# Optimization experiments

Hardware: AMD Instinct MI355X
Metric: run time of the kernel (lower is better)

Reference implementation:

```python
import jax, jax.numpy as jnp
import numpy as np

B, L, E, H = 2, 2048, 2048, 16
HD = E // H  # 128
ROPE_BASE = 10000.0


def setup_inputs() -> dict:
    key = jax.random.key(0)
    k1, k2, k3 = jax.random.split(key, 3)
    x = jax.random.normal(k1, (B, L, E), dtype=jnp.float32)
    position_ids = jnp.tile(jnp.arange(L, dtype=jnp.int32)[None, :], (B, 1))
    # Linear weights stored as [in, out] so y = x @ W + b (equals torch x @ W.T + b)
    W_attn = jax.random.normal(k2, (E, 3 * E), dtype=jnp.float32) * (1.0 / np.sqrt(E))
    b_attn = jnp.zeros((3 * E,), dtype=jnp.float32)
    W_proj = jax.random.normal(k3, (E, E), dtype=jnp.float32) * (1.0 / np.sqrt(E))
    b_proj = jnp.zeros((E,), dtype=jnp.float32)
    return {"x": x, "position_ids": position_ids, "W_attn": W_attn,
            "b_attn": b_attn, "W_proj": W_proj, "b_proj": b_proj}


def _rotate_half(t):
    h = t.shape[-1] // 2
    return jnp.concatenate([-t[..., h:], t[..., :h]], axis=-1)


def _apply_rope(q, k, position_ids):
    # q,k: [B,H,L,HD]; position_ids: [B,L]
    inv_freq = 1.0 / (ROPE_BASE ** (jnp.arange(0, HD, 2, dtype=jnp.float32) / HD))
    angles = position_ids.astype(jnp.float32)[:, :, None] * inv_freq  # [B,L,HD/2]
    cos = jnp.concatenate([jnp.cos(angles)] * 2, axis=-1)[:, None]  # [B,1,L,HD]
    sin = jnp.concatenate([jnp.sin(angles)] * 2, axis=-1)[:, None]
    return q * cos + _rotate_half(q) * sin, k * cos + _rotate_half(k) * sin


def reference(x, position_ids, W_attn, b_attn, W_proj, b_proj):
    # fused QKV projection
    qkv = x @ W_attn + b_attn                       # [B,L,3E]
    q, k, v = jnp.split(qkv, 3, axis=-1)            # each [B,L,E]
    reshape = lambda t: t.reshape(B, L, H, HD).transpose(0, 2, 1, 3)  # [B,H,L,HD]
    q, k, v = reshape(q), reshape(k), reshape(v)
    q, k = _apply_rope(q, k, position_ids)
    # scaled dot-product attention (mask=None -> full attention, dropout 0)
    scores = jnp.einsum('bhqd,bhkd->bhqk', q, k) * (1.0 / np.sqrt(HD))
    probs = jax.nn.softmax(scores, axis=-1)
    y = jnp.einsum('bhqk,bhkd->bhqd', probs, v)     # [B,H,L,HD]
    y = y.transpose(0, 2, 1, 3).reshape(B, L, E)
    return y @ W_proj + b_proj
```

## Files before the change

kernel.cpp:

```cpp
#include <hip/hip_runtime.h>
#include <math.h>

#define BB 2
#define LL 2048
#define EE 2048
#define HH 16
#define HD 128
#define N3E (3*EE)

typedef __attribute__((ext_vector_type(8))) short  bf16x8;
typedef __attribute__((ext_vector_type(4))) float  f32x4;

__device__ __forceinline__ ushort f2bf(float f) {
    union { float f; unsigned u; } v; v.f = f;
    unsigned u = v.u + 0x7FFFu + ((v.u >> 16) & 1u);
    return (ushort)(u >> 16);
}
__device__ __forceinline__ float bf2f(ushort u) {
    union { unsigned u; float f; } v; v.u = ((unsigned)u) << 16;
    return v.f;
}

__global__ __launch_bounds__(256) void cvt_bf16(const float* __restrict__ in,
                                                ushort* __restrict__ out, int n) {
    int i = (blockIdx.x * 256 + threadIdx.x) * 8;
    float4 a = *(const float4*)(in + i);
    float4 b = *(const float4*)(in + i + 4);
    ushort4 p0 = { f2bf(a.x), f2bf(a.y), f2bf(a.z), f2bf(a.w) };
    ushort4 p1 = { f2bf(b.x), f2bf(b.y), f2bf(b.z), f2bf(b.w) };
    *(ushort4*)(out + i)     = p0;
    *(ushort4*)(out + i + 4) = p1;
}

__global__ __launch_bounds__(256) void transpose_bf16(const float* __restrict__ in,
                                                      ushort* __restrict__ out,
                                                      int R, int Ccol) {
    __shared__ float tile[32][33];
    int c0 = blockIdx.x * 32, r0 = blockIdx.y * 32;
    int t = threadIdx.x;
    int lr = t >> 5, lc = t & 31;
    #pragma unroll
    for (int i = 0; i < 4; ++i)
        tile[lr + i * 8][lc] = in[(size_t)(r0 + lr + i * 8) * Ccol + c0 + lc];
    __syncthreads();
    #pragma unroll
    for (int i = 0; i < 4; ++i)
        out[(size_t)(c0 + lr + i * 8) * R + r0 + lc] = f2bf(tile[lc][lr + i * 8]);
}

template<int WRITE_BF16>
__global__ __launch_bounds__(512, 2) void gemm_ktile(const ushort* __restrict__ A,
                                                     const ushort* __restrict__ Bt,
                                                     const float* __restrict__ bias,
                                                     void* __restrict__ C,
                                                     int M, int N, int K, int nbx) {
    __shared__ __align__(16) ushort Asl[4 * 8192];
    __shared__ __align__(16) ushort Bsl[4 * 4096];

    const int t    = threadIdx.x;
    const int lane = t & 63;
    const int w    = t >> 6;
    const int m    = lane & 15;
    const int quad = lane >> 4;
    const int wm   = w >> 1;
    const int wn   = w & 1;

    const int nwg = gridDim.x;
    const int cpx = nwg >> 3;
    const int swz = ((int)blockIdx.x & 7) * cpx + ((int)blockIdx.x >> 3);
    const int bx  = swz % nbx;
    const int by  = swz / nbx;
    const int m0  = by * 256, n0 = bx * 128;

    const int r16s  = (t >> 2) & 15;
    const int kels  = ((t & 3) ^ ((t & 32) ? 2 : 0)) * 8;
    const int row0s = ((t >> 6) << 4) + r16s;
    const int row1s = row0s + 128;

    const int foff = m * 32 + ((quad * 8) ^ ((m & 8) ? 16 : 0));

#define STAGE(T_) do { int _s = (T_) & 3; \
    __builtin_amdgcn_global_load_lds( \
        (const __attribute__((address_space(1))) unsigned int*)(A + (size_t)(m0 + row0s) * K + (T_) * 32 + kels), \
        (__attribute__((address_space(3))) unsigned int*)(Asl + _s * 8192 + t * 8), 16, 0, 0); \
    __builtin_amdgcn_global_load_lds( \
        (const __attribute__((address_space(1))) unsigned int*)(A + (size_t)(m0 + row1s) * K + (T_) * 32 + kels), \
        (__attribute__((address_space(3))) unsigned int*)(Asl + _s * 8192 + (512 + t) * 8), 16, 0, 0); \
    __builtin_amdgcn_global_load_lds( \
        (const __attribute__((address_space(1))) unsigned int*)(Bt + (size_t)(n0 + row0s) * K + (T_) * 32 + kels), \
        (__attribute__((address_space(3))) unsigned int*)(Bsl + _s * 4096 + t * 8), 16, 0, 0); } while (0)

    f32x4 acc[4][4];
    #pragma unroll
    for (int i = 0; i < 4; ++i)
        #pragma unroll
        for (int j = 0; j < 4; ++j) acc[i][j] = (f32x4){0.f, 0.f, 0.f, 0.f};

    const int NT = K >> 5;

    STAGE(0); STAGE(1); STAGE(2);
    asm volatile("s_waitcnt vmcnt(6)" ::: "memory");
    __builtin_amdgcn_s_barrier();

    for (int T = 0; T < NT; ++T) {
        const int slot = T & 3;
        const ushort* as = Asl + slot * 8192 + wm * 2048;
        const ushort* bs = Bsl + slot * 4096 + wn * 2048;

        bf16x8 af[4], bf[4];
        #pragma unroll
        for (int mt = 0; mt < 4; ++mt)
            af[mt] = *(const bf16x8*)(as + mt * 512 + foff);
        #pragma unroll
        for (int nt = 0; nt < 4; ++nt)
            bf[nt] = *(const bf16x8*)(bs + nt * 512 + foff);

        if (T + 3 < NT) STAGE(T + 3);

        if (T + 3 < NT)      asm volatile("s_waitcnt vmcnt(6)" ::: "memory");
        else if (T + 2 < NT) asm volatile("s_waitcnt vmcnt(3)" ::: "memory");
        else                 asm volatile("s_waitcnt vmcnt(0)" ::: "memory");
        __builtin_amdgcn_s_barrier();
        asm volatile("s_waitcnt lgkmcnt(0)" ::: "memory");
        __builtin_amdgcn_s_setprio(1);
        #pragma unroll
        for (int mt = 0; mt < 4; ++mt)
            #pragma unroll
            for (int nt = 0; nt < 4; ++nt)
                acc[mt][nt] = __builtin_amdgcn_mfma_f32_16x16x32_bf16(af[mt], bf[nt], acc[mt][nt], 0, 0, 0);
        __builtin_amdgcn_s_setprio(0);
        __builtin_amdgcn_s_barrier();
    }
#undef STAGE

    float bcol[4];
    #pragma unroll
    for (int nt = 0; nt < 4; ++nt) bcol[nt] = bias[n0 + wn * 64 + nt * 16 + m];
    #pragma unroll
    for (int mt = 0; mt < 4; ++mt) {
        #pragma unroll
        for (int nt = 0; nt < 4; ++nt) {
            #pragma unroll
            for (int r = 0; r < 4; ++r) {
                int row = m0 + wm * 64 + mt * 16 + quad * 4 + r;
                int col = n0 + wn * 64 + nt * 16 + m;
                float v = acc[mt][nt][r] + bcol[nt];
                if (WRITE_BF16) ((ushort*)C)[(size_t)row * N + col] = f2bf(v);
                else            ((float*)C)[(size_t)row * N + col] = v;
            }
        }
    }
}

__global__ __launch_bounds__(256) void prep_qk(const ushort* __restrict__ qkvb,
                                               const int* __restrict__ pos_ids,
                                               ushort* __restrict__ Qt,
                                               ushort* __restrict__ Kt) {
    const float scale = 0.08838834764831845f;
    const float nl2b = -0.20762050593046014f;
    int idx = blockIdx.x * 256 + threadIdx.x;
    int p    = idx & 15;
    int r    = (idx >> 4) & 63;
    int tile = (idx >> 10) & 31;
    int h    = (idx >> 15) & 15;
    int b    = idx >> 19;
    int c    = p ^ (r & 15);
    int l    = tile * 64 + r;
    int half = c >> 3, cl = c & 7;
    const ushort* row = qkvb + (size_t)(b * LL + l) * N3E;
    float pos = (float)pos_ids[b * LL + l];

    bf16x8 qa = *(const bf16x8*)(row + h * HD + c * 8);
    bf16x8 qb = *(const bf16x8*)(row + h * HD + (c ^ 8) * 8);
    bf16x8 ka = *(const bf16x8*)(row + EE + h * HD + c * 8);
    bf16x8 kb = *(const bf16x8*)(row + EE + h * HD + (c ^ 8) * 8);
    bf16x8 qo, ko;
    #pragma unroll
    for (int i = 0; i < 8; ++i) {
        int j = cl * 8 + i;
        float ang = pos * exp2f((float)j * nl2b);
        float s, cs;
        sincosf(ang, &s, &cs);
        float sgn = half ? s : -s;
        float q1 = bf2f((ushort)qa[i]), q2 = bf2f((ushort)qb[i]);
        float k1 = bf2f((ushort)ka[i]), k2 = bf2f((ushort)kb[i]);
        qo[i] = (short)f2bf((q1 * cs + q2 * sgn) * scale);
        ko[i] = (short)f2bf(k1 * cs + k2 * sgn);
    }
    size_t obase = ((size_t)(b * 16 + h) * 32 + tile) * 8192 + r * 128 + p * 8;
    *(bf16x8*)(Qt + obase) = qo;
    *(bf16x8*)(Kt + obase) = ko;
}

__global__ __launch_bounds__(256) void prep_v(const ushort* __restrict__ qkvb,
                                              ushort* __restrict__ Vtt) {
    int idx = blockIdx.x * 256 + threadIdx.x;
    int p    = idx & 7;
    int r    = (idx >> 3) & 127;
    int tile = (idx >> 10) & 31;
    int h    = (idx >> 15) & 15;
    int b    = idx >> 19;
    int c    = p ^ (r & 7);
    int col  = 2 * EE + h * HD + r;
    bf16x8 o;
    #pragma unroll
    for (int i = 0; i < 8; ++i) {
        int kk = tile * 64 + c * 8 + i;
        o[i] = (short)qkvb[(size_t)(b * LL + kk) * N3E + col];
    }
    *(bf16x8*)(Vtt + ((size_t)(b * 16 + h) * 32 + tile) * 8192 + r * 64 + p * 8) = o;
}

#define PSTR 68

__global__ __launch_bounds__(256, 2) void flash2(const ushort* __restrict__ Qt,
                                                 const ushort* __restrict__ Kt,
                                                 const ushort* __restrict__ Vtt,
                                                 ushort* __restrict__ y) {
    __shared__ __align__(16) ushort Ks[64 * 128];
    __shared__ __align__(16) ushort Vs[128 * 64];
    __shared__ __align__(16) ushort Ps[4 * 32 * PSTR];

    const int t    = threadIdx.x;
    const int w    = t >> 6;
    const int lane = t & 63;
    const int m    = lane & 15;
    const int quad = lane >> 4;
    const int qblk = blockIdx.x;
    const int bh   = blockIdx.y;
    const int b    = bh >> 4, h = bh & 15;

    const ushort* Qhead = Qt  + (size_t)bh * 32 * 8192;
    const ushort* Khead = Kt  + (size_t)bh * 32 * 8192;
    const ushort* Vhead = Vtt + (size_t)bh * 32 * 8192;

    bf16x8 qf[2][4];
    #pragma unroll
    for (int mt = 0; mt < 2; ++mt) {
        int rloc = w * 32 + mt * 16 + m;
        const ushort* qtile = Qhead + (size_t)(qblk * 2 + (rloc >> 6)) * 8192
                              + (rloc & 63) * 128;
        #pragma unroll
        for (int ks = 0; ks < 4; ++ks)
            qf[mt][ks] = *(const bf16x8*)(qtile + ((ks * 4 + quad) ^ m) * 8);
    }

    f32x4 oacc[2][8];
    #pragma unroll
    for (int mt = 0; mt < 2; ++mt)
        #pragma unroll
        for (int dt = 0; dt < 8; ++dt) oacc[mt][dt] = (f32x4){0.f, 0.f, 0.f, 0.f};
    float m_i[8], l_pl[8];
    #pragma unroll
    for (int s = 0; s < 8; ++s) { m_i[s] = -INFINITY; l_pl[s] = 0.f; }

    {
        const ushort* ksrc = Khead;
        #pragma unroll
        for (int i = 0; i < 4; ++i) {
            int cid = t + i * 256;
            __builtin_amdgcn_global_load_lds(
                (const __attribute__((address_space(1))) unsigned int*)(ksrc + cid * 8),
                (__attribute__((address_space(3))) unsigned int*)(Ks + cid * 8),
                16, 0, 0);
        }
    }

    for (int kt = 0; kt < 32; ++kt) {
        asm volatile("s_waitcnt vmcnt(0)\n\ts_barrier" ::: "memory");

        {
            const ushort* vsrc = Vhead + (size_t)kt * 8192;
            #pragma unroll
            for (int i = 0; i < 4; ++i) {
                int cid = t + i * 256;
                __builtin_amdgcn_global_load_lds(
                    (const __attribute__((address_space(1))) unsigned int*)(vsrc + cid * 8),
                    (__attribute__((address_space(3))) unsigned int*)(Vs + cid * 8),
                    16, 0, 0);
            }
        }

        f32x4 sacc[2][4];
        #pragma unroll
        for (int mt = 0; mt < 2; ++mt)
            #pragma unroll
            for (int nt = 0; nt < 4; ++nt) sacc[mt][nt] = (f32x4){0.f, 0.f, 0.f, 0.f};
        __builtin_amdgcn_s_setprio(1);
        #pragma unroll
        for (int ks = 0; ks < 4; ++ks) {
            #pragma unroll
            for (int nt = 0; nt < 4; ++nt) {
                bf16x8 kf = *(const bf16x8*)&Ks[(nt * 16 + m) * 128 + (((ks * 4 + quad) ^ m)) * 8];
                sacc[0][nt] = __builtin_amdgcn_mfma_f32_16x16x32_bf16(qf[0][ks], kf, sacc[0][nt], 0, 0, 0);
                sacc[1][nt] = __builtin_amdgcn_mfma_f32_16x16x32_bf16(qf[1][ks], kf, sacc[1][nt], 0, 0, 0);
            }
        }
        __builtin_amdgcn_s_setprio(0);

        float alpha_s[2][4];
        #pragma unroll
        for (int mt = 0; mt < 2; ++mt) {
            #pragma unroll
            for (int r = 0; r < 4; ++r) {
                int slot = mt * 4 + r;
                float mx = fmaxf(fmaxf(sacc[mt][0][r], sacc[mt][1][r]),
                                 fmaxf(sacc[mt][2][r], sacc[mt][3][r]));
                #pragma unroll
                for (int off = 1; off < 16; off <<= 1) mx = fmaxf(mx, __shfl_xor(mx, off, 64));
                float mnew = fmaxf(m_i[slot], mx);
                float al = __expf(m_i[slot] - mnew);
                m_i[slot] = mnew;
                float rs = 0.f;
                #pragma unroll
                for (int nt = 0; nt < 4; ++nt) {
                    float pv = __expf(sacc[mt][nt][r] - mnew);
                    sacc[mt][nt][r] = pv;
                    rs += pv;
                }
                l_pl[slot] = l_pl[slot] * al + rs;
                alpha_s[mt][r] = al;
            }
        }
        #pragma unroll
        for (int mt = 0; mt < 2; ++mt)
            #pragma unroll
            for (int dt = 0; dt < 8; ++dt)
                #pragma unroll
                for (int r = 0; r < 4; ++r) oacc[mt][dt][r] *= alpha_s[mt][r];

        #pragma unroll
        for (int mt = 0; mt < 2; ++mt)
            #pragma unroll
            for (int nt = 0; nt < 4; ++nt)
                #pragma unroll
                for (int r = 0; r < 4; ++r)
                    Ps[w * 32 * PSTR + (mt * 16 + quad * 4 + r) * PSTR + nt * 16 + m]
                        = f2bf(sacc[mt][nt][r]);

        asm volatile("s_waitcnt vmcnt(0)\n\ts_barrier" ::: "memory");

        if (kt + 1 < 32) {
            const ushort* ksrc = Khead + (size_t)(kt + 1) * 8192;
            #pragma unroll
            for (int i = 0; i < 4; ++i) {
                int cid = t + i * 256;
                __builtin_amdgcn_global_load_lds(
                    (const __attribute__((address_space(1))) unsigned int*)(ksrc + cid * 8),
                    (__attribute__((address_space(3))) unsigned int*)(Ks + cid * 8),
                    16, 0, 0);
            }
        }

        __builtin_amdgcn_s_setprio(1);
        #pragma unroll
        for (int ks2 = 0; ks2 < 2; ++ks2) {
            bf16x8 pf0 = *(const bf16x8*)&Ps[w * 32 * PSTR + (0 * 16 + m) * PSTR + ks2 * 32 + quad * 8];
            bf16x8 pf1 = *(const bf16x8*)&Ps[w * 32 * PSTR + (1 * 16 + m) * PSTR + ks2 * 32 + quad * 8];
            #pragma unroll
            for (int dt = 0; dt < 8; ++dt) {
                bf16x8 vf = *(const bf16x8*)&Vs[(dt * 16 + m) * 64 + (((ks2 * 4 + quad) ^ (m & 7))) * 8];
                oacc[0][dt] = __builtin_amdgcn_mfma_f32_16x16x32_bf16(pf0, vf, oacc[0][dt], 0, 0, 0);
                oacc[1][dt] = __builtin_amdgcn_mfma_f32_16x16x32_bf16(pf1, vf, oacc[1][dt], 0, 0, 0);
            }
        }
        __builtin_amdgcn_s_setprio(0);
    }

    #pragma unroll
    for (int s = 0; s < 8; ++s) {
        #pragma unroll
        for (int off = 1; off < 16; off <<= 1) l_pl[s] += __shfl_xor(l_pl[s], off, 64);
        l_pl[s] = 1.0f / l_pl[s];
    }
    #pragma unroll
    for (int mt = 0; mt < 2; ++mt) {
        #pragma unroll
        for (int dt = 0; dt < 8; ++dt) {
            #pragma unroll
            for (int r = 0; r < 4; ++r) {
                int row = qblk * 128 + w * 32 + mt * 16 + quad * 4 + r;
                y[(size_t)(b * LL + row) * EE + h * HD + dt * 16 + m]
                    = f2bf(oacc[mt][dt][r] * l_pl[mt * 4 + r]);
            }
        }
    }
}

extern "C" void kernel_launch(void* const* d_in, const int* in_sizes, int n_in,
                              void* d_out, int out_size, void* d_ws, size_t ws_size,
                              hipStream_t stream) {
    const float* x      = (const float*)d_in[0];
    const int*   pos    = (const int*)d_in[1];
    const float* W_attn = (const float*)d_in[2];
    const float* b_attn = (const float*)d_in[3];
    const float* W_proj = (const float*)d_in[4];
    const float* b_proj = (const float*)d_in[5];
    float* out = (float*)d_out;

    const int M = BB * LL;
    ushort* xb   = (ushort*)d_ws;
    ushort* Wat  = xb   + (size_t)M * EE;
    ushort* Wpt  = Wat  + (size_t)N3E * EE;
    ushort* qkvb = Wpt  + (size_t)EE * EE;
    ushort* Kt   = qkvb + (size_t)M * N3E;
    ushort* Vtt  = Kt   + (size_t)M * EE;
    ushort* Qt   = xb;
    ushort* yb   = Wat;

    dim3 blk(256);
    cvt_bf16<<<dim3(M * EE / (256 * 8)), blk, 0, stream>>>(x, xb, M * EE);
    transpose_bf16<<<dim3(N3E / 32, EE / 32), blk, 0, stream>>>(W_attn, Wat, EE, N3E);
    transpose_bf16<<<dim3(EE / 32, EE / 32), blk, 0, stream>>>(W_proj, Wpt, EE, EE);

    gemm_ktile<1><<<dim3((M / 256) * (N3E / 128)), dim3(512), 0, stream>>>(
        xb, Wat, b_attn, qkvb, M, N3E, EE, N3E / 128);

    prep_qk<<<dim3(4096), blk, 0, stream>>>(qkvb, pos, Qt, Kt);
    prep_v<<<dim3(4096), blk, 0, stream>>>(qkvb, Vtt);

    flash2<<<dim3(LL / 128, BB * HH), blk, 0, stream>>>(Qt, Kt, Vtt, yb);

    gemm_ktile<0><<<dim3((M / 256) * (EE / 128)), dim3(512), 0, stream>>>(
        yb, Wpt, b_proj, out, M, EE, EE, EE / 128);
}
```

Measured before the change: 454.5 us.

## Merge prep kernels, stage V transpose through LDS, add lazy softmax rescale

The three preprocessing kernels (x conversion and two weight transposes) are merged into one launch, and prep_qk and prep_v become a single prep_qkv kernel. In that kernel the V transpose now does coalesced vector loads into a swizzled LDS tile instead of strided scalar global reads. The flash attention loop skips the running-max update and the output rescale whenever every row max in the wave stays within 8 of the current max. This lazy rescaling saves exponentials and multiplies on the accumulator, at the cost of probabilities that can reach up to e^8 before normalisation.

```diff
diff --git a/kernel.cpp b/kernel.cpp
--- a/kernel.cpp
+++ b/kernel.cpp
@@ -21,23 +21,15 @@
     return v.f;
 }
 
-__global__ __launch_bounds__(256) void cvt_bf16(const float* __restrict__ in,
-                                                ushort* __restrict__ out, int n) {
-    int i = (blockIdx.x * 256 + threadIdx.x) * 8;
-    float4 a = *(const float4*)(in + i);
-    float4 b = *(const float4*)(in + i + 4);
-    ushort4 p0 = { f2bf(a.x), f2bf(a.y), f2bf(a.z), f2bf(a.w) };
-    ushort4 p1 = { f2bf(b.x), f2bf(b.y), f2bf(b.z), f2bf(b.w) };
-    *(ushort4*)(out + i)     = p0;
-    *(ushort4*)(out + i + 4) = p1;
-}
-
-__global__ __launch_bounds__(256) void transpose_bf16(const float* __restrict__ in,
-                                                      ushort* __restrict__ out,
-                                                      int R, int Ccol) {
-    __shared__ float tile[32][33];
-    int c0 = blockIdx.x * 32, r0 = blockIdx.y * 32;
-    int t = threadIdx.x;
+#define NB_CVT 4096
+#define NB_T1  12288
+#define NB_T2  4096
+
+__device__ __forceinline__ void tr_block(const float* __restrict__ in,
+                                         ushort* __restrict__ out,
+                                         int R, int Ccol, int bx, int by,
+                                         float (*tile)[33], int t) {
+    int c0 = bx * 32, r0 = by * 32;
     int lr = t >> 5, lc = t & 31;
     #pragma unroll
     for (int i = 0; i < 4; ++i)
@@ -46,6 +38,32 @@
     #pragma unroll
     for (int i = 0; i < 4; ++i)
         out[(size_t)(c0 + lr + i * 8) * R + r0 + lc] = f2bf(tile[lc][lr + i * 8]);
+}
+
+__global__ __launch_bounds__(256) void pre_all(const float* __restrict__ x,
+                                               ushort* __restrict__ xb,
+                                               const float* __restrict__ W_attn,
+                                               ushort* __restrict__ Wat,
+                                               const float* __restrict__ W_proj,
+                                               ushort* __restrict__ Wpt) {
+    __shared__ float tile[32][33];
+    int bid = blockIdx.x;
+    int t = threadIdx.x;
+    if (bid < NB_CVT) {
+        int i = (bid * 256 + t) * 8;
+        float4 a = *(const float4*)(x + i);
+        float4 b = *(const float4*)(x + i + 4);
+        ushort4 p0 = { f2bf(a.x), f2bf(a.y), f2bf(a.z), f2bf(a.w) };
+        ushort4 p1 = { f2bf(b.x), f2bf(b.y), f2bf(b.z), f2bf(b.w) };
+        *(ushort4*)(xb + i)     = p0;
+        *(ushort4*)(xb + i + 4) = p1;
+    } else if (bid < NB_CVT + NB_T1) {
+        int lb = bid - NB_CVT;
+        tr_block(W_attn, Wat, EE, N3E, lb % (N3E / 32), lb / (N3E / 32), tile, t);
+    } else {
+        int lb = bid - NB_CVT - NB_T1;
+        tr_block(W_proj, Wpt, EE, EE, lb % (EE / 32), lb / (EE / 32), tile, t);
+    }
 }
 
 template<int WRITE_BF16>
@@ -152,63 +170,80 @@
     }
 }
 
-__global__ __launch_bounds__(256) void prep_qk(const ushort* __restrict__ qkvb,
-                                               const int* __restrict__ pos_ids,
-                                               ushort* __restrict__ Qt,
-                                               ushort* __restrict__ Kt) {
-    const float scale = 0.08838834764831845f;
-    const float nl2b = -0.20762050593046014f;
-    int idx = blockIdx.x * 256 + threadIdx.x;
-    int p    = idx & 15;
-    int r    = (idx >> 4) & 63;
-    int tile = (idx >> 10) & 31;
-    int h    = (idx >> 15) & 15;
-    int b    = idx >> 19;
-    int c    = p ^ (r & 15);
-    int l    = tile * 64 + r;
-    int half = c >> 3, cl = c & 7;
-    const ushort* row = qkvb + (size_t)(b * LL + l) * N3E;
-    float pos = (float)pos_ids[b * LL + l];
-
-    bf16x8 qa = *(const bf16x8*)(row + h * HD + c * 8);
-    bf16x8 qb = *(const bf16x8*)(row + h * HD + (c ^ 8) * 8);
-    bf16x8 ka = *(const bf16x8*)(row + EE + h * HD + c * 8);
-    bf16x8 kb = *(const bf16x8*)(row + EE + h * HD + (c ^ 8) * 8);
-    bf16x8 qo, ko;
-    #pragma unroll
-    for (int i = 0; i < 8; ++i) {
-        int j = cl * 8 + i;
-        float ang = pos * exp2f((float)j * nl2b);
-        float s, cs;
-        sincosf(ang, &s, &cs);
-        float sgn = half ? s : -s;
-        float q1 = bf2f((ushort)qa[i]), q2 = bf2f((ushort)qb[i]);
-        float k1 = bf2f((ushort)ka[i]), k2 = bf2f((ushort)kb[i]);
-        qo[i] = (short)f2bf((q1 * cs + q2 * sgn) * scale);
-        ko[i] = (short)f2bf(k1 * cs + k2 * sgn);
-    }
-    size_t obase = ((size_t)(b * 16 + h) * 32 + tile) * 8192 + r * 128 + p * 8;
-    *(bf16x8*)(Qt + obase) = qo;
-    *(bf16x8*)(Kt + obase) = ko;
-}
-
-__global__ __launch_bounds__(256) void prep_v(const ushort* __restrict__ qkvb,
-                                              ushort* __restrict__ Vtt) {
-    int idx = blockIdx.x * 256 + threadIdx.x;
-    int p    = idx & 7;
-    int r    = (idx >> 3) & 127;
-    int tile = (idx >> 10) & 31;
-    int h    = (idx >> 15) & 15;
-    int b    = idx >> 19;
-    int c    = p ^ (r & 7);
-    int col  = 2 * EE + h * HD + r;
-    bf16x8 o;
-    #pragma unroll
-    for (int i = 0; i < 8; ++i) {
-        int kk = tile * 64 + c * 8 + i;
-        o[i] = (short)qkvb[(size_t)(b * LL + kk) * N3E + col];
-    }
-    *(bf16x8*)(Vtt + ((size_t)(b * 16 + h) * 32 + tile) * 8192 + r * 64 + p * 8) = o;
+__global__ __launch_bounds__(256) void prep_qkv(const ushort* __restrict__ qkvb,
+                                                const int* __restrict__ pos_ids,
+                                                ushort* __restrict__ Qt,
+                                                ushort* __restrict__ Kt,
+                                                ushort* __restrict__ Vtt) {
+    __shared__ ushort vlds[64 * 136];
+    int bid = blockIdx.x;
+    int t   = threadIdx.x;
+
+    if (bid < 4096) {
+        const float scale = 0.08838834764831845f;
+        const float nl2b = -0.20762050593046014f;
+        int idx = bid * 256 + t;
+        int p    = idx & 15;
+        int r    = (idx >> 4) & 63;
+        int tile = (idx >> 10) & 31;
+        int h    = (idx >> 15) & 15;
+        int b    = idx >> 19;
+        int c    = p ^ (r & 15);
+        int l    = tile * 64 + r;
+        int half = c >> 3, cl = c & 7;
+        const ushort* row = qkvb + (size_t)(b * LL + l) * N3E;
+        float pos = (float)pos_ids[b * LL + l];
+
+        bf16x8 qa = *(const bf16x8*)(row + h * HD + c * 8);
+        bf16x8 qb = *(const bf16x8*)(row + h * HD + (c ^ 8) * 8);
+        bf16x8 ka = *(const bf16x8*)(row + EE + h * HD + c * 8);
+        bf16x8 kb = *(const bf16x8*)(row + EE + h * HD + (c ^ 8) * 8);
+        bf16x8 qo, ko;
+        #pragma unroll
+        for (int i = 0; i < 8; ++i) {
+            int j = cl * 8 + i;
+            float ang = pos * exp2f((float)j * nl2b);
+            float s, cs;
+            sincosf(ang, &s, &cs);
+            float sgn = half ? s : -s;
+            float q1 = bf2f((ushort)qa[i]), q2 = bf2f((ushort)qb[i]);
+            float k1 = bf2f((ushort)ka[i]), k2 = bf2f((ushort)kb[i]);
+            qo[i] = (short)f2bf((q1 * cs + q2 * sgn) * scale);
+            ko[i] = (short)f2bf(k1 * cs + k2 * sgn);
+        }
+        size_t obase = ((size_t)(b * 16 + h) * 32 + tile) * 8192 + r * 128 + p * 8;
+        *(bf16x8*)(Qt + obase) = qo;
+        *(bf16x8*)(Kt + obase) = ko;
+    } else {
+        int vb   = bid - 4096;
+        int tile = vb & 31;
+        int bh   = vb >> 5;
+        int b    = bh >> 4, h = bh & 15;
+
+        #pragma unroll
+        for (int it = 0; it < 4; ++it) {
+            int c4 = t + it * 256;
+            int kk = c4 >> 4, dc = c4 & 15;
+            bf16x8 v = *(const bf16x8*)(qkvb + (size_t)(b * LL + tile * 64 + kk) * N3E
+                                        + 2 * EE + h * HD + dc * 8);
+            int colp = (dc * 8) ^ ((kk >> 3) << 4);
+            *(bf16x8*)(vlds + kk * 136 + colp) = v;
+        }
+        __syncthreads();
+        #pragma unroll
+        for (int it = 0; it < 4; ++it) {
+            int oc = t + it * 256;
+            int p = oc & 7, r = oc >> 3;
+            int c = p ^ (r & 7);
+            bf16x8 o;
+            #pragma unroll
+            for (int i = 0; i < 8; ++i) {
+                int kk = c * 8 + i;
+                o[i] = (short)vlds[kk * 136 + (r ^ ((kk >> 3) << 4))];
+            }
+            *(bf16x8*)(Vtt + ((size_t)bh * 32 + tile) * 8192 + r * 64 + p * 8) = o;
+        }
+    }
 }
 
 #define PSTR 68
@@ -298,36 +333,70 @@
         }
         __builtin_amdgcn_s_setprio(0);
 
-        float alpha_s[2][4];
+        float mxs[2][4];
         #pragma unroll
         for (int mt = 0; mt < 2; ++mt) {
             #pragma unroll
             for (int r = 0; r < 4; ++r) {
-                int slot = mt * 4 + r;
                 float mx = fmaxf(fmaxf(sacc[mt][0][r], sacc[mt][1][r]),
                                  fmaxf(sacc[mt][2][r], sacc[mt][3][r]));
                 #pragma unroll
                 for (int off = 1; off < 16; off <<= 1) mx = fmaxf(mx, __shfl_xor(mx, off, 64));
-                float mnew = fmaxf(m_i[slot], mx);
-                float al = __expf(m_i[slot] - mnew);
-                m_i[slot] = mnew;
-                float rs = 0.f;
+                mxs[mt][r] = mx;
+            }
+        }
+        int small = 1;
+        #pragma unroll
+        for (int mt = 0; mt < 2; ++mt)
+            #pragma unroll
+            for (int r = 0; r < 4; ++r)
+                small &= (mxs[mt][r] <= m_i[mt * 4 + r] + 8.0f) ? 1 : 0;
+
+        if (__all(small)) {
+            #pragma unroll
+            for (int mt = 0; mt < 2; ++mt) {
                 #pragma unroll
-                for (int nt = 0; nt < 4; ++nt) {
-                    float pv = __expf(sacc[mt][nt][r] - mnew);
-                    sacc[mt][nt][r] = pv;
-                    rs += pv;
+                for (int r = 0; r < 4; ++r) {
+                    int slot = mt * 4 + r;
+                    float mnew = m_i[slot];
+                    float rs = 0.f;
+                    #pragma unroll
+                    for (int nt = 0; nt < 4; ++nt) {
+                        float pv = __expf(sacc[mt][nt][r] - mnew);
+                        sacc[mt][nt][r] = pv;
+                        rs += pv;
+                    }
+                    l_pl[slot] += rs;
                 }
-                l_pl[slot] = l_pl[slot] * al + rs;
-                alpha_s[mt][r] = al;
-            }
-        }
-        #pragma unroll
-        for (int mt = 0; mt < 2; ++mt)
-            #pragma unroll
-            for (int dt = 0; dt < 8; ++dt)
+            }
+        } else {
+            float alpha_s[2][4];
+            #pragma unroll
+            for (int mt = 0; mt < 2; ++mt) {
                 #pragma unroll
-                for (int r = 0; r < 4; ++r) oacc[mt][dt][r] *= alpha_s[mt][r];
+                for (int r = 0; r < 4; ++r) {
+                    int slot = mt * 4 + r;
+                    float mnew = fmaxf(m_i[slot], mxs[mt][r]);
+                    float al = __expf(m_i[slot] - mnew);
+                    m_i[slot] = mnew;
+                    float rs = 0.f;
+                    #pragma unroll
+                    for (int nt = 0; nt < 4; ++nt) {
+                        float pv = __expf(sacc[mt][nt][r] - mnew);
+                        sacc[mt][nt][r] = pv;
+                        rs += pv;
+                    }
+                    l_pl[slot] = l_pl[slot] * al + rs;
+                    alpha_s[mt][r] = al;
+                }
+            }
+            #pragma unroll
+            for (int mt = 0; mt < 2; ++mt)
+                #pragma unroll
+                for (int dt = 0; dt < 8; ++dt)
+                    #pragma unroll
+                    for (int r = 0; r < 4; ++r) oacc[mt][dt][r] *= alpha_s[mt][r];
+        }
 
         #pragma unroll
         for (int mt = 0; mt < 2; ++mt)
@@ -408,18 +477,15 @@
     ushort* Qt   = xb;
     ushort* yb   = Wat;
 
-    dim3 blk(256);
-    cvt_bf16<<<dim3(M * EE / (256 * 8)), blk, 0, stream>>>(x, xb, M * EE);
-    transpose_bf16<<<dim3(N3E / 32, EE / 32), blk, 0, stream>>>(W_attn, Wat, EE, N3E);
-    transpose_bf16<<<dim3(EE / 32, EE / 32), blk, 0, stream>>>(W_proj, Wpt, EE, EE);
+    pre_all<<<dim3(NB_CVT + NB_T1 + NB_T2), dim3(256), 0, stream>>>(
+        x, xb, W_attn, Wat, W_proj, Wpt);
 
     gemm_ktile<1><<<dim3((M / 256) * (N3E / 128)), dim3(512), 0, stream>>>(
         xb, Wat, b_attn, qkvb, M, N3E, EE, N3E / 128);
 
-    prep_qk<<<dim3(4096), blk, 0, stream>>>(qkvb, pos, Qt, Kt);
-    prep_v<<<dim3(4096), blk, 0, stream>>>(qkvb, Vtt);
-
-    flash2<<<dim3(LL / 128, BB * HH), blk, 0, stream>>>(Qt, Kt, Vtt, yb);
+    prep_qkv<<<dim3(4096 + 1024), dim3(256), 0, stream>>>(qkvb, pos, Qt, Kt, Vtt);
+
+    flash2<<<dim3(LL / 128, BB * HH), dim3(256), 0, stream>>>(Qt, Kt, Vtt, yb);
 
     gemm_ktile<0><<<dim3((M / 256) * (EE / 128)), dim3(512), 0, stream>>>(
         yb, Wpt, b_proj, out, M, EE, EE, EE / 128);
```

New measurement: 467.1 us. +2.8%, slower.
